# Optimization experiments

Hardware: AMD Instinct MI355X
Metric: run time of the kernel (lower is better)

Reference implementation:

```python
import jax, jax.numpy as jnp
import numpy as np

IN_DIM = 768
ATT_DIM = 512
N_HEADS = 8
HEAD_DIM = ATT_DIM // N_HEADS


def setup_inputs() -> dict:
    key = jax.random.key(0)
    k1, k2, k3 = jax.random.split(key, 3)
    X = jax.random.normal(k1, (4, 2048, IN_DIM), dtype=jnp.float32)
    # qkv linear (no bias): weight [3*att_dim, in_dim], torch convention y = x W^T
    W_qkv = jax.random.normal(k2, (3 * ATT_DIM, IN_DIM), dtype=jnp.float32) * (1.0 / np.sqrt(IN_DIM))
    W_out = jax.random.normal(k3, (IN_DIM, ATT_DIM), dtype=jnp.float32) * (1.0 / np.sqrt(ATT_DIM))
    b_out = jnp.zeros((IN_DIM,), dtype=jnp.float32)
    return {"X": X, "W_qkv": W_qkv, "W_out": W_out, "b_out": b_out}


def reference(X, W_qkv, W_out, b_out):
    b, n, _ = X.shape
    QKV = jnp.einsum('bnf,cf->bnc', X, W_qkv)  # [b, n, 3*att_dim]
    # rearrange 'b n (p h d) -> p b h n d'
    QKV = QKV.reshape(b, n, 3, N_HEADS, HEAD_DIM).transpose(2, 0, 3, 1, 4)
    Q, K, V = QKV[0], QKV[1], QKV[2]  # each [b, h, n, d]
    scores = jnp.einsum('bhid,bhjd->bhij', Q, K) / np.sqrt(HEAD_DIM)
    A = jax.nn.softmax(scores, axis=-1)  # dropout p=0 -> identity
    Y = jnp.einsum('bhij,bhjd->bhid', A, V)
    Y = Y.transpose(0, 2, 1, 3).reshape(b, n, ATT_DIM)  # 'b h n d -> b n (h d)'
    return jnp.einsum('bna,oa->bno', Y, W_out) + b_out
```

## Files before the change

### kernel.cpp

```cpp
#include <hip/hip_runtime.h>

typedef __bf16 bf16;
typedef unsigned int u32;
typedef __attribute__((ext_vector_type(8))) __bf16 bf16x8;
typedef __attribute__((ext_vector_type(4))) __bf16 bf16x4;
typedef __attribute__((ext_vector_type(4))) float floatx4;
typedef __attribute__((ext_vector_type(16))) float floatx16;
typedef __attribute__((ext_vector_type(4))) int int4v;

#define IN_DIM  768
#define ATT_DIM 512
#define NH      8
#define HD      64
#define BATCH   4
#define SEQ     2048
#define M_TOT   (BATCH*SEQ)
#define QKV_N   (3*ATT_DIM)

#define QSCALE 0.18033688011112042f

__device__ __forceinline__ void cp16(void* lds, const void* g) {
    __builtin_amdgcn_global_load_lds((const __attribute__((address_space(1))) u32*)g,
                                     (__attribute__((address_space(3))) u32*)lds, 16, 0, 0);
}
__device__ __forceinline__ const bf16* swz(const bf16* b, int row, int chunk) {
    return b + row * 64 + (((chunk) ^ (row & 7)) << 3);
}
__device__ __forceinline__ bf16x8 ld_swz8(const bf16* tile, int row, int chunk) {
    const char* base = (const char*)(tile + row * 64) + (((chunk ^ (row & 7)) << 4));
    const int off = row & 8;
    const bf16x4 h0 = *(const bf16x4*)(base + off);
    const bf16x4 h1 = *(const bf16x4*)(base + (off ^ 8));
    return (bf16x8){h0[0], h0[1], h0[2], h0[3], h1[0], h1[1], h1[2], h1[3]};
}

__device__ __forceinline__ int cvtpk_bf16(float lo, float hi) {
    int r;
    asm("v_cvt_pk_bf16_f32 %0, %1, %2" : "=v"(r) : "v"(lo), "v"(hi));
    return r;
}
__device__ __forceinline__ void plswap(int& a, int& b) {
    asm("v_permlane32_swap_b32 %0, %1" : "+v"(a), "+v"(b));
}

#define N8_X  (M_TOT * IN_DIM / 8)
#define N8_WQ (QKV_N * IN_DIM / 8)
#define N8_WO (IN_DIM * ATT_DIM / 8)
#define N8_ALL (N8_X + N8_WQ + N8_WO)

__global__ __launch_bounds__(256) void cvt_all(const float* __restrict__ X,
                                               const float* __restrict__ Wq,
                                               const float* __restrict__ Wo,
                                               bf16* __restrict__ Xb,
                                               bf16* __restrict__ Wqb,
                                               bf16* __restrict__ Wob) {
    int i = blockIdx.x * 256 + threadIdx.x;
    const float* s; bf16* d; int off;
    if (i < N8_X)            { s = X;  d = Xb;  off = i; }
    else if (i < N8_X+N8_WQ) { s = Wq; d = Wqb; off = i - N8_X; }
    else                     { s = Wo; d = Wob; off = i - N8_X - N8_WQ; }
    const float4 a = ((const float4*)s)[2*off];
    const float4 b = ((const float4*)s)[2*off+1];
    bf16x8 o = {(bf16)a.x,(bf16)a.y,(bf16)a.z,(bf16)a.w,
                (bf16)b.x,(bf16)b.y,(bf16)b.z,(bf16)b.w};
    ((bf16x8*)d)[off] = o;
}

__global__ __launch_bounds__(256) void qkv_gemm(const bf16* __restrict__ Xb,
                                                const bf16* __restrict__ Wb,
                                                bf16* __restrict__ Q,
                                                bf16* __restrict__ Kv,
                                                bf16* __restrict__ VT) {
    __shared__ __align__(16) char smraw[34816];
    bf16* As = (bf16*)smraw;
    bf16* Bs = (bf16*)(smraw + 16384);

    const int tid  = threadIdx.x;
    const int bm0  = blockIdx.y * 128;
    const int bn0  = blockIdx.x * 128;
    const int wave = tid >> 6, lane = tid & 63;
    const int quad = lane >> 4, l15 = lane & 15;
    const int wm = (wave >> 1) * 64, wn = (wave & 1) * 64;
    const int r8 = lane >> 3, cc = (lane & 7) ^ r8;

    const bf16* ag = Xb + (size_t)(bm0 + wave * 32 + r8) * IN_DIM + cc * 8;
    const bf16* bg = Wb + (size_t)(bn0 + wave * 32 + r8) * IN_DIM + cc * 8;

    floatx4 acc[4][4];
#pragma unroll
    for (int i = 0; i < 4; ++i)
#pragma unroll
        for (int j = 0; j < 4; ++j) acc[i][j] = (floatx4){0.f, 0.f, 0.f, 0.f};

    for (int kt = 0; kt < IN_DIM / 64; ++kt) {
        __syncthreads();
#pragma unroll
        for (int it = 0; it < 4; ++it) {
            cp16(&As[(wave * 32 + it * 8) * 64], ag + it * (8 * IN_DIM) + kt * 64);
            cp16(&Bs[(wave * 32 + it * 8) * 64], bg + it * (8 * IN_DIM) + kt * 64);
        }
        __syncthreads();

        bf16x8 af[2][4], bfr[2][4];
#pragma unroll
        for (int kh = 0; kh < 2; ++kh)
#pragma unroll
            for (int i = 0; i < 4; ++i) {
                af[kh][i]  = *(const bf16x8*)swz(As, wm + i * 16 + l15, kh * 4 + quad);
                bfr[kh][i] = *(const bf16x8*)swz(Bs, wn + i * 16 + l15, kh * 4 + quad);
            }
#pragma unroll
        for (int kh = 0; kh < 2; ++kh)
#pragma unroll
            for (int i = 0; i < 4; ++i)
#pragma unroll
                for (int j = 0; j < 4; ++j)
                    acc[i][j] = __builtin_amdgcn_mfma_f32_16x16x32_bf16(af[kh][i], bfr[kh][j], acc[i][j], 0, 0, 0);
    }

    const int b = bm0 >> 11, nbase = bm0 & 2047;

    if (bn0 < 512) {
#pragma unroll
        for (int i = 0; i < 4; ++i)
#pragma unroll
            for (int j = 0; j < 4; ++j)
#pragma unroll
                for (int r = 0; r < 4; ++r) {
                    const int row = bm0 + wm + i * 16 + quad * 4 + r;
                    const int col = bn0 + wn + j * 16 + l15;
                    const int h = col >> 6, d = col & 63;
                    const int n = row & 2047;
                    const size_t idx = (((size_t)((row >> 11) * NH + h)) * SEQ + n) * HD + d;
                    Q[idx] = (bf16)(acc[i][j][r] * QSCALE);
                }
    } else if (bn0 < 1024) {
#pragma unroll
        for (int i = 0; i < 4; ++i)
#pragma unroll
            for (int j = 0; j < 4; ++j)
#pragma unroll
                for (int r = 0; r < 4; ++r) {
                    const int row = bm0 + wm + i * 16 + quad * 4 + r;
                    const int col = bn0 - 512 + wn + j * 16 + l15;
                    const int h = col >> 6, d = col & 63;
                    const int n = row & 2047;
                    const size_t idx = (((size_t)((row >> 11) * NH + h)) * SEQ + n) * HD + d;
                    Kv[idx ^ (size_t)((n >> 1) & 4)] = (bf16)acc[i][j][r];
                }
    } else {
        __syncthreads();
        bf16 (*Ts)[136] = (bf16(*)[136])smraw;
#pragma unroll
        for (int i = 0; i < 4; ++i)
#pragma unroll
            for (int j = 0; j < 4; ++j) {
                bf16x4 pk = {(bf16)acc[i][j][0], (bf16)acc[i][j][1],
                             (bf16)acc[i][j][2], (bf16)acc[i][j][3]};
                *(bf16x4*)&Ts[wn + j * 16 + l15][wm + i * 16 + quad * 4] = pk;
            }
        __syncthreads();
        const int cb = bn0 - 1024;
#pragma unroll
        for (int t2 = 0; t2 < 8; ++t2) {
            const int id = tid + t2 * 256;
            const int c = id >> 4, nc = (id & 15) * 8;
            const int col = cb + c;
            const int h = col >> 6, d = col & 63;
            bf16x8 val = *(const bf16x8*)&Ts[c][nc];
            if (d & 8)
                val = __builtin_shufflevector(val, val, 4, 5, 6, 7, 0, 1, 2, 3);
            *(bf16x8*)&VT[(((size_t)(b * NH + h)) * HD + d) * SEQ + nbase + nc] = val;
        }
    }
}

__global__ __launch_bounds__(256, 2) void attn(const bf16* __restrict__ Q,
                                               const bf16* __restrict__ K,
                                               const bf16* __restrict__ VT,
                                               bf16* __restrict__ Y) {
    __shared__ bf16 Ks[2][64 * 64];
    __shared__ bf16 VTs[2][64 * 64];

    const int tid  = threadIdx.x;
    const int wave = tid >> 6, lane = tid & 63;
    const int l31  = lane & 31, hi = lane >> 5;
    const int bh = blockIdx.x;
    const int q0 = blockIdx.y * 128;
    const bf16* Qg = Q  + (size_t)bh * SEQ * HD;
    const bf16* Kg = K  + (size_t)bh * SEQ * HD;
    const bf16* Vg = VT + (size_t)bh * HD * SEQ;

    bf16x8 aq[4];
    {
        const bf16* qrow = Qg + (size_t)(q0 + wave * 32 + l31) * HD;
#pragma unroll
        for (int c = 0; c < 4; ++c)
            aq[c] = *(const bf16x8*)(qrow + c * 16 + hi * 8);
    }

    const int r8 = lane >> 3, cc8 = (lane & 7) ^ r8;
    const bf16* kgw = Kg + (size_t)(wave * 16 + r8) * HD + cc8 * 8;
    const bf16* vgw = Vg + (size_t)(wave * 16 + r8) * SEQ + cc8 * 8;

    float l = 0.f;
    floatx16 oa[2], ob[2];
#pragma unroll
    for (int i = 0; i < 16; ++i) {
        oa[0][i] = 0.f; oa[1][i] = 0.f;
        ob[0][i] = 0.f; ob[1][i] = 0.f;
    }

#pragma unroll
    for (int it = 0; it < 2; ++it) {
        cp16(&Ks[0][(wave * 16 + it * 8) * 64], kgw + (size_t)(it * 8) * HD);
        cp16(&VTs[0][(wave * 16 + it * 8) * 64], vgw + (size_t)(it * 8) * SEQ);
    }

    for (int kt = 0; kt < SEQ / 64; ++kt) {
        const int cur = kt & 1;
        __syncthreads();
        if (kt < SEQ / 64 - 1) {
#pragma unroll
            for (int it = 0; it < 2; ++it) {
                cp16(&Ks[cur ^ 1][(wave * 16 + it * 8) * 64],
                     kgw + (size_t)((kt + 1) * 64 + it * 8) * HD);
                cp16(&VTs[cur ^ 1][(wave * 16 + it * 8) * 64],
                     vgw + (size_t)(it * 8) * SEQ + (kt + 1) * 64);
            }
        }

#pragma unroll
        for (int kb = 0; kb < 2; ++kb) {
            const int krow = kb * 32 + l31;
            bf16x8 kf[4];
#pragma unroll
            for (int c = 0; c < 4; ++c)
                kf[c] = ld_swz8(Ks[cur], krow, c * 2 + hi);
            bf16x8 vf[2][2];
#pragma unroll
            for (int db = 0; db < 2; ++db) {
                vf[db][0] = ld_swz8(VTs[cur], db * 32 + l31, kb * 4 + hi);
                vf[db][1] = ld_swz8(VTs[cur], db * 32 + l31, kb * 4 + 2 + hi);
            }

            floatx16 s0, s1;
#pragma unroll
            for (int i = 0; i < 16; ++i) { s0[i] = 0.f; s1[i] = 0.f; }
            __builtin_amdgcn_s_setprio(1);
            s0 = __builtin_amdgcn_mfma_f32_32x32x16_bf16(kf[0], aq[0], s0, 0, 0, 0);
            s1 = __builtin_amdgcn_mfma_f32_32x32x16_bf16(kf[1], aq[1], s1, 0, 0, 0);
            s0 = __builtin_amdgcn_mfma_f32_32x32x16_bf16(kf[2], aq[2], s0, 0, 0, 0);
            s1 = __builtin_amdgcn_mfma_f32_32x32x16_bf16(kf[3], aq[3], s1, 0, 0, 0);
            __builtin_amdgcn_s_setprio(0);
            float p[16];
#pragma unroll
            for (int i = 0; i < 16; ++i)
                p[i] = __builtin_amdgcn_exp2f(s0[i] + s1[i]);
            {
                const float t0 = (p[0] + p[1]) + (p[2] + p[3]);
                const float t1 = (p[4] + p[5]) + (p[6] + p[7]);
                const float t2 = (p[8] + p[9]) + (p[10] + p[11]);
                const float t3 = (p[12] + p[13]) + (p[14] + p[15]);
                l += (t0 + t1) + (t2 + t3);
            }
            int w[8];
#pragma unroll
            for (int i = 0; i < 8; ++i) w[i] = cvtpk_bf16(p[2 * i], p[2 * i + 1]);
            plswap(w[0], w[2]); plswap(w[1], w[3]);
            plswap(w[4], w[6]); plswap(w[5], w[7]);
            const int4v f0i = {w[0], w[1], w[2], w[3]};
            const int4v f1i = {w[4], w[5], w[6], w[7]};
            const bf16x8 f0 = __builtin_bit_cast(bf16x8, f0i);
            const bf16x8 f1 = __builtin_bit_cast(bf16x8, f1i);
            __builtin_amdgcn_s_setprio(1);
#pragma unroll
            for (int db = 0; db < 2; ++db) {
                oa[db] = __builtin_amdgcn_mfma_f32_32x32x16_bf16(f0, vf[db][0], oa[db], 0, 0, 0);
                ob[db] = __builtin_amdgcn_mfma_f32_32x32x16_bf16(f1, vf[db][1], ob[db], 0, 0, 0);
            }
            __builtin_amdgcn_s_setprio(0);
        }
    }

    l += __shfl_xor(l, 32, 64);
    const float inv = 1.0f / l;
    const int b = bh >> 3, h = bh & 7;
#pragma unroll
    for (int reg = 0; reg < 16; ++reg) {
        const int qr = (reg & 3) + 8 * (reg >> 2) + 4 * hi;
        const float li = __int_as_float(
            __builtin_amdgcn_ds_bpermute(qr << 2, __float_as_int(inv)));
        const int n = q0 + wave * 32 + qr;
        bf16* yrow = Y + ((size_t)(b * SEQ + n)) * ATT_DIM + h * HD + l31;
        yrow[0]  = (bf16)((oa[0][reg] + ob[0][reg]) * li);
        yrow[32] = (bf16)((oa[1][reg] + ob[1][reg]) * li);
    }
}

__global__ __launch_bounds__(256) void out_gemm(const bf16* __restrict__ Yb,
                                                const bf16* __restrict__ Wb,
                                                const float* __restrict__ bias,
                                                float* __restrict__ out) {
    __shared__ __align__(16) bf16 As[128 * 64];
    __shared__ __align__(16) bf16 Bs[128 * 64];

    const int tid  = threadIdx.x;
    const int bm0  = blockIdx.y * 128;
    const int bn0  = blockIdx.x * 128;
    const int wave = tid >> 6, lane = tid & 63;
    const int quad = lane >> 4, l15 = lane & 15;
    const int wm = (wave >> 1) * 64, wn = (wave & 1) * 64;
    const int r8 = lane >> 3, cc = (lane & 7) ^ r8;

    const bf16* ag = Yb + (size_t)(bm0 + wave * 32 + r8) * ATT_DIM + cc * 8;
    const bf16* bg = Wb + (size_t)(bn0 + wave * 32 + r8) * ATT_DIM + cc * 8;

    floatx4 acc[4][4];
#pragma unroll
    for (int i = 0; i < 4; ++i)
#pragma unroll
        for (int j = 0; j < 4; ++j) acc[i][j] = (floatx4){0.f, 0.f, 0.f, 0.f};

    for (int kt = 0; kt < ATT_DIM / 64; ++kt) {
        __syncthreads();
#pragma unroll
        for (int it = 0; it < 4; ++it) {
            cp16(&As[(wave * 32 + it * 8) * 64], ag + it * (8 * ATT_DIM) + kt * 64);
            cp16(&Bs[(wave * 32 + it * 8) * 64], bg + it * (8 * ATT_DIM) + kt * 64);
        }
        __syncthreads();

        bf16x8 af[2][4], bfr[2][4];
#pragma unroll
        for (int kh = 0; kh < 2; ++kh)
#pragma unroll
            for (int i = 0; i < 4; ++i) {
                af[kh][i]  = *(const bf16x8*)swz(As, wm + i * 16 + l15, kh * 4 + quad);
                bfr[kh][i] = *(const bf16x8*)swz(Bs, wn + i * 16 + l15, kh * 4 + quad);
            }
#pragma unroll
        for (int kh = 0; kh < 2; ++kh)
#pragma unroll
            for (int i = 0; i < 4; ++i)
#pragma unroll
                for (int j = 0; j < 4; ++j)
                    acc[i][j] = __builtin_amdgcn_mfma_f32_16x16x32_bf16(af[kh][i], bfr[kh][j], acc[i][j], 0, 0, 0);
    }

#pragma unroll
    for (int i = 0; i < 4; ++i)
#pragma unroll
        for (int j = 0; j < 4; ++j)
#pragma unroll
            for (int r = 0; r < 4; ++r) {
                const int row = bm0 + wm + i * 16 + quad * 4 + r;
                const int col = bn0 + wn + j * 16 + l15;
                out[(size_t)row * IN_DIM + col] = acc[i][j][r] + bias[col];
            }
}

extern "C" void kernel_launch(void* const* d_in, const int* in_sizes, int n_in,
                              void* d_out, int out_size, void* d_ws, size_t ws_size,
                              hipStream_t stream) {
    const float* X    = (const float*)d_in[0];
    const float* Wqkv = (const float*)d_in[1];
    const float* Wout = (const float*)d_in[2];
    const float* bout = (const float*)d_in[3];
    float* out = (float*)d_out;

    char* ws = (char*)d_ws;
    size_t off = 0;
    bf16* Xb  = (bf16*)(ws + off); off += (size_t)M_TOT * IN_DIM * 2;
    bf16* Wqb = (bf16*)(ws + off); off += (size_t)QKV_N * IN_DIM * 2;
    bf16* Wob = (bf16*)(ws + off); off += (size_t)IN_DIM * ATT_DIM * 2;
    const size_t T = (size_t)BATCH * NH * SEQ * HD * 2;
    bf16* Q  = (bf16*)(ws + off); off += T;
    bf16* K  = (bf16*)(ws + off); off += T;
    bf16* VT = (bf16*)(ws + off); off += T;
    bf16* Y  = (bf16*)(ws + off); off += T;

    cvt_all<<<N8_ALL / 256, 256, 0, stream>>>(X, Wqkv, Wout, Xb, Wqb, Wob);
    qkv_gemm<<<dim3(QKV_N / 128, M_TOT / 128), 256, 0, stream>>>(Xb, Wqb, Q, K, VT);
    attn<<<dim3(BATCH * NH, SEQ / 128), 256, 0, stream>>>(Q, K, VT, Y);
    out_gemm<<<dim3(IN_DIM / 128, M_TOT / 128), 256, 0, stream>>>(Y, Wob, bout, out);
}
```

Before: 175.0 us.

## Remap GEMM blocks per XCD and cut attention accumulators for higher occupancy

Both GEMMs now remap the linear block id so consecutive tiles go to the same XCD (id&7 round-robin inverted), aiming for better L2 reuse of shared A/B tiles. The attention kernel merges its split accumulators (s0/s1, oa/ob) into single chains, lowering register use, and raises launch bounds from 2 to 4 blocks per CU. The price is longer dependent MFMA chains, which latency hiding from the extra occupancy has to cover.

```diff
diff --git a/kernel.cpp b/kernel.cpp
--- a/kernel.cpp
+++ b/kernel.cpp
@@ -76,8 +76,10 @@
     bf16* Bs = (bf16*)(smraw + 16384);
 
     const int tid  = threadIdx.x;
-    const int bm0  = blockIdx.y * 128;
-    const int bn0  = blockIdx.x * 128;
+    const int id  = blockIdx.y * 12 + blockIdx.x;
+    const int nid = (id & 7) * 96 + (id >> 3);
+    const int bm0 = (nid / 12) * 128;
+    const int bn0 = (nid % 12) * 128;
     const int wave = tid >> 6, lane = tid & 63;
     const int quad = lane >> 4, l15 = lane & 15;
     const int wm = (wave >> 1) * 64, wn = (wave & 1) * 64;
@@ -163,8 +165,8 @@
         const int cb = bn0 - 1024;
 #pragma unroll
         for (int t2 = 0; t2 < 8; ++t2) {
-            const int id = tid + t2 * 256;
-            const int c = id >> 4, nc = (id & 15) * 8;
+            const int id2 = tid + t2 * 256;
+            const int c = id2 >> 4, nc = (id2 & 15) * 8;
             const int col = cb + c;
             const int h = col >> 6, d = col & 63;
             bf16x8 val = *(const bf16x8*)&Ts[c][nc];
@@ -175,7 +177,7 @@
     }
 }
 
-__global__ __launch_bounds__(256, 2) void attn(const bf16* __restrict__ Q,
+__global__ __launch_bounds__(256, 4) void attn(const bf16* __restrict__ Q,
                                                const bf16* __restrict__ K,
                                                const bf16* __restrict__ VT,
                                                bf16* __restrict__ Y) {
@@ -204,12 +206,9 @@
     const bf16* vgw = Vg + (size_t)(wave * 16 + r8) * SEQ + cc8 * 8;
 
     float l = 0.f;
-    floatx16 oa[2], ob[2];
-#pragma unroll
-    for (int i = 0; i < 16; ++i) {
-        oa[0][i] = 0.f; oa[1][i] = 0.f;
-        ob[0][i] = 0.f; ob[1][i] = 0.f;
-    }
+    floatx16 o[2];
+#pragma unroll
+    for (int i = 0; i < 16; ++i) { o[0][i] = 0.f; o[1][i] = 0.f; }
 
 #pragma unroll
     for (int it = 0; it < 2; ++it) {
@@ -244,19 +243,17 @@
                 vf[db][1] = ld_swz8(VTs[cur], db * 32 + l31, kb * 4 + 2 + hi);
             }
 
-            floatx16 s0, s1;
-#pragma unroll
-            for (int i = 0; i < 16; ++i) { s0[i] = 0.f; s1[i] = 0.f; }
+            floatx16 s;
+#pragma unroll
+            for (int i = 0; i < 16; ++i) s[i] = 0.f;
             __builtin_amdgcn_s_setprio(1);
-            s0 = __builtin_amdgcn_mfma_f32_32x32x16_bf16(kf[0], aq[0], s0, 0, 0, 0);
-            s1 = __builtin_amdgcn_mfma_f32_32x32x16_bf16(kf[1], aq[1], s1, 0, 0, 0);
-            s0 = __builtin_amdgcn_mfma_f32_32x32x16_bf16(kf[2], aq[2], s0, 0, 0, 0);
-            s1 = __builtin_amdgcn_mfma_f32_32x32x16_bf16(kf[3], aq[3], s1, 0, 0, 0);
+#pragma unroll
+            for (int c = 0; c < 4; ++c)
+                s = __builtin_amdgcn_mfma_f32_32x32x16_bf16(kf[c], aq[c], s, 0, 0, 0);
             __builtin_amdgcn_s_setprio(0);
             float p[16];
 #pragma unroll
-            for (int i = 0; i < 16; ++i)
-                p[i] = __builtin_amdgcn_exp2f(s0[i] + s1[i]);
+            for (int i = 0; i < 16; ++i) p[i] = __builtin_amdgcn_exp2f(s[i]);
             {
                 const float t0 = (p[0] + p[1]) + (p[2] + p[3]);
                 const float t1 = (p[4] + p[5]) + (p[6] + p[7]);
@@ -276,8 +273,8 @@
             __builtin_amdgcn_s_setprio(1);
 #pragma unroll
             for (int db = 0; db < 2; ++db) {
-                oa[db] = __builtin_amdgcn_mfma_f32_32x32x16_bf16(f0, vf[db][0], oa[db], 0, 0, 0);
-                ob[db] = __builtin_amdgcn_mfma_f32_32x32x16_bf16(f1, vf[db][1], ob[db], 0, 0, 0);
+                o[db] = __builtin_amdgcn_mfma_f32_32x32x16_bf16(f0, vf[db][0], o[db], 0, 0, 0);
+                o[db] = __builtin_amdgcn_mfma_f32_32x32x16_bf16(f1, vf[db][1], o[db], 0, 0, 0);
             }
             __builtin_amdgcn_s_setprio(0);
         }
@@ -293,8 +290,8 @@
             __builtin_amdgcn_ds_bpermute(qr << 2, __float_as_int(inv)));
         const int n = q0 + wave * 32 + qr;
         bf16* yrow = Y + ((size_t)(b * SEQ + n)) * ATT_DIM + h * HD + l31;
-        yrow[0]  = (bf16)((oa[0][reg] + ob[0][reg]) * li);
-        yrow[32] = (bf16)((oa[1][reg] + ob[1][reg]) * li);
+        yrow[0]  = (bf16)(o[0][reg] * li);
+        yrow[32] = (bf16)(o[1][reg] * li);
     }
 }
 
@@ -306,8 +303,10 @@
     __shared__ __align__(16) bf16 Bs[128 * 64];
 
     const int tid  = threadIdx.x;
-    const int bm0  = blockIdx.y * 128;
-    const int bn0  = blockIdx.x * 128;
+    const int id  = blockIdx.y * 6 + blockIdx.x;
+    const int nid = (id & 7) * 48 + (id >> 3);
+    const int bm0 = (nid / 6) * 128;
+    const int bn0 = (nid % 6) * 128;
     const int wave = tid >> 6, lane = tid & 63;
     const int quad = lane >> 4, l15 = lane & 15;
     const int wm = (wave >> 1) * 64, wn = (wave & 1) * 64;
```

After: 167.0 us. 4.6% less time.
